# Kernel tuning notes

Measured on AMD Instinct MI355X. Metric: run time of the kernel, lower is better.

## Reference

```python
import jax, jax.numpy as jnp
import numpy as np

N, E = 50000, 500000
D_NODE, D_EDGE, N_REL, N_CLS = 128, 128, 64, 16


def setup_inputs() -> dict:
    key = jax.random.key(0)
    ks = jax.random.split(key, 16)
    cat = 2 * D_NODE + D_EDGE  # 384
    s = 0.05
    return {
        "node_features": jax.random.normal(ks[0], (N, D_NODE), jnp.float32),
        "edge_features": jax.random.normal(ks[1], (E, D_EDGE), jnp.float32),
        "edge_index": jax.random.randint(ks[2], (2, E), 0, N, jnp.int32),
        "labels_for_rel_emb": jax.random.randint(ks[3], (E,), 0, N_REL, jnp.int32),
        "rel_emb": jax.random.normal(ks[4], (N_REL, D_EDGE), jnp.float32) * s,
        "msg_W": jax.random.normal(ks[5], (D_NODE, cat), jnp.float32) * s,
        "msg_b": jnp.zeros((D_NODE,), jnp.float32),
        "gru_w_ih": jax.random.normal(ks[6], (3 * D_NODE, D_NODE), jnp.float32) * s,
        "gru_w_hh": jax.random.normal(ks[7], (3 * D_NODE, D_NODE), jnp.float32) * s,
        "gru_b_ih": jnp.zeros((3 * D_NODE,), jnp.float32),
        "gru_b_hh": jnp.zeros((3 * D_NODE,), jnp.float32),
        "cls_W1": jax.random.normal(ks[8], (D_EDGE, cat), jnp.float32) * s,
        "cls_b1": jnp.zeros((D_EDGE,), jnp.float32),
        "cls_W2": jax.random.normal(ks[9], (N_CLS, D_EDGE), jnp.float32) * s,
        "cls_b2": jnp.zeros((N_CLS,), jnp.float32),
    }


def reference(node_features, edge_features, edge_index, labels_for_rel_emb,
              rel_emb, msg_W, msg_b, gru_w_ih, gru_w_hh, gru_b_ih, gru_b_hh,
              cls_W1, cls_b1, cls_W2, cls_b2):
    src, tgt = edge_index[0], edge_index[1]
    nf = node_features
    rel_feat = rel_emb[labels_for_rel_emb]                      # [E, d_edge]
    h = jnp.concatenate([nf[src], nf[tgt], rel_feat], axis=-1)  # [E, 384]
    msg = jax.nn.gelu(h @ msg_W.T + msg_b, approximate=False)   # [E, d_node]
    agg = jax.ops.segment_sum(msg, tgt, num_segments=nf.shape[0])  # [N, d_node]
    # torch.nn.GRUCell(agg, nf)
    gi = agg @ gru_w_ih.T + gru_b_ih
    gh = nf @ gru_w_hh.T + gru_b_hh
    i_r, i_z, i_n = jnp.split(gi, 3, axis=-1)
    h_r, h_z, h_n = jnp.split(gh, 3, axis=-1)
    r = jax.nn.sigmoid(i_r + h_r)
    z = jax.nn.sigmoid(i_z + h_z)
    n = jnp.tanh(i_n + r * h_n)
    nf_u = (1.0 - z) * n + z * nf
    c = jnp.concatenate([nf_u[src], nf_u[tgt], edge_features], axis=-1)  # [E, 384]
    hc = jax.nn.gelu(c @ cls_W1.T + cls_b1, approximate=False)           # [E, d_edge]
    return hc @ cls_W2.T + cls_b2                                        # [E, num_classes]
```

## Files before the change

kernel.cpp:

```cpp
#include <hip/hip_runtime.h>
#include <math.h>

#define N_NODES 50000
#define N_EDGES 500000
#define D 128
#define CAT 384

typedef __bf16 v8bf __attribute__((ext_vector_type(8)));
typedef __bf16 v2bf __attribute__((ext_vector_type(2)));
typedef float v4f __attribute__((ext_vector_type(4)));

__device__ __forceinline__ float erf_fast(float x) {
    float ax = fabsf(x);
    float t = __builtin_amdgcn_rcpf(fmaf(0.3275911f, ax, 1.0f));
    float p = fmaf(1.061405429f, t, -1.453152027f);
    p = fmaf(p, t, 1.421413741f);
    p = fmaf(p, t, -0.284496736f);
    p = fmaf(p, t, 0.254829592f);
    p = p * t;
    float e = __expf(-ax * ax);
    float r = 1.0f - p * e;
    return copysignf(r, x);
}

__device__ __forceinline__ float gelu_fast(float x) {
    return 0.5f * x * (1.0f + erf_fast(x * 0.70710678118654752440f));
}

__device__ __forceinline__ float sigmoid_fast(float x) {
    float e = __expf(-x);
    return __builtin_amdgcn_rcpf(1.0f + e);
}

__device__ __forceinline__ float tanh_fast(float x) {
    float e = __expf(2.0f * x);
    return 1.0f - 2.0f * __builtin_amdgcn_rcpf(e + 1.0f);
}

__device__ __forceinline__ v8bf cvt8(const float* __restrict__ p) {
    float4 f0 = *(const float4*)p;
    float4 f1 = *(const float4*)(p + 4);
    v8bf r;
    r[0] = (__bf16)f0.x; r[1] = (__bf16)f0.y; r[2] = (__bf16)f0.z; r[3] = (__bf16)f0.w;
    r[4] = (__bf16)f1.x; r[5] = (__bf16)f1.y; r[6] = (__bf16)f1.z; r[7] = (__bf16)f1.w;
    return r;
}

__global__ __launch_bounds__(256) void k_cvtw(const float* __restrict__ msgW,
                                              const float* __restrict__ W1,
                                              const float* __restrict__ W2,
                                              const float* __restrict__ wih,
                                              const float* __restrict__ whh,
                                              __bf16* __restrict__ WB) {
    int i = blockIdx.x * 256 + threadIdx.x;
    float v;
    if (i < 32768) {
        int j = i >> 7, k = i & 127;
        v = (j < 128) ? msgW[j * CAT + k] : msgW[(j - 128) * CAT + 128 + k];
    } else if (i < 65536) {
        int ii = i - 32768; int j = ii >> 7, k = ii & 127;
        v = (j < 128) ? W1[j * CAT + k] : W1[(j - 128) * CAT + 128 + k];
    } else if (i < 81920) {
        int ii = i - 65536; int j = ii >> 7, k = ii & 127;
        v = W1[j * CAT + 256 + k];
    } else if (i < 83968) {
        v = W2[i - 81920];
    } else if (i < 133120) {
        v = wih[i - 83968];
    } else {
        v = whh[i - 133120];
    }
    WB[i] = (__bf16)v;
}

__global__ void k_relpart(const float* __restrict__ rel_emb,
                          const float* __restrict__ msg_W,
                          const float* __restrict__ msg_b,
                          __bf16* __restrict__ RPB) {
    int r = blockIdx.x;
    int j = threadIdx.x;
    const float* er = rel_emb + r * D;
    const float* wr = msg_W + j * CAT + 2 * D;
    float acc = msg_b[j];
    #pragma unroll 8
    for (int k = 0; k < D; ++k) acc += er[k] * wr[k];
    RPB[r * D + j] = (__bf16)acc;
}

__global__ __launch_bounds__(256) void k_proj2_f32(const float* __restrict__ in,
                                                   const __bf16* __restrict__ wb,
                                                   __bf16* __restrict__ out) {
    int t = threadIdx.x;
    int lane = t & 63, wid = t >> 6;
    int g = lane >> 4, c = lane & 15;
    int nbase = blockIdx.x * 64 + wid * 16;

    int nrow = min(nbase + c, N_NODES - 1);
    const float* ir = in + (size_t)nrow * D + g * 8;
    v8bf afrag[4];
    #pragma unroll
    for (int kc = 0; kc < 4; ++kc) afrag[kc] = cvt8(ir + kc * 32);

    #pragma unroll
    for (int half = 0; half < 2; ++half) {
        v4f acc[8];
        #pragma unroll 2
        for (int jt = 0; jt < 8; ++jt) {
            const __bf16* wr = wb + (size_t)(half * 128 + 8 * c + jt) * 128 + g * 8;
            v4f a4 = (v4f){0.f, 0.f, 0.f, 0.f};
            #pragma unroll
            for (int kc = 0; kc < 4; ++kc)
                a4 = __builtin_amdgcn_mfma_f32_16x16x32_bf16(afrag[kc], *(const v8bf*)(wr + kc * 32), a4, 0, 0, 0);
            acc[jt] = a4;
        }
        #pragma unroll
        for (int r = 0; r < 4; ++r) {
            int node = nbase + g * 4 + r;
            v8bf o;
            #pragma unroll
            for (int jt = 0; jt < 8; ++jt) o[jt] = (__bf16)acc[jt][r];
            if (node < N_NODES)
                *(v8bf*)(out + (size_t)node * 256 + half * 128 + 8 * c) = o;
        }
    }
}

__global__ __launch_bounds__(256) void k_proj2_b16(const __bf16* __restrict__ in,
                                                   const __bf16* __restrict__ wb,
                                                   __bf16* __restrict__ out) {
    int t = threadIdx.x;
    int lane = t & 63, wid = t >> 6;
    int g = lane >> 4, c = lane & 15;
    int nbase = blockIdx.x * 64 + wid * 16;

    int nrow = min(nbase + c, N_NODES - 1);
    const __bf16* ir = in + (size_t)nrow * D + g * 8;
    v8bf afrag[4];
    #pragma unroll
    for (int kc = 0; kc < 4; ++kc) afrag[kc] = *(const v8bf*)(ir + kc * 32);

    #pragma unroll
    for (int half = 0; half < 2; ++half) {
        v4f acc[8];
        #pragma unroll 2
        for (int jt = 0; jt < 8; ++jt) {
            const __bf16* wr = wb + (size_t)(half * 128 + 8 * c + jt) * 128 + g * 8;
            v4f a4 = (v4f){0.f, 0.f, 0.f, 0.f};
            #pragma unroll
            for (int kc = 0; kc < 4; ++kc)
                a4 = __builtin_amdgcn_mfma_f32_16x16x32_bf16(afrag[kc], *(const v8bf*)(wr + kc * 32), a4, 0, 0, 0);
            acc[jt] = a4;
        }
        #pragma unroll
        for (int r = 0; r < 4; ++r) {
            int node = nbase + g * 4 + r;
            v8bf o;
            #pragma unroll
            for (int jt = 0; jt < 8; ++jt) o[jt] = (__bf16)acc[jt][r];
            if (node < N_NODES)
                *(v8bf*)(out + (size_t)node * 256 + half * 128 + 8 * c) = o;
        }
    }
}

__global__ __launch_bounds__(256) void k_hist(const int* __restrict__ ei,
                                              int* __restrict__ counts) {
    int e = blockIdx.x * 256 + threadIdx.x;
    if (e < N_EDGES) atomicAdd(&counts[ei[N_EDGES + e]], 1);
}

__global__ __launch_bounds__(256) void k_scan(const int* __restrict__ counts,
                                              int* __restrict__ offsets,
                                              int* __restrict__ cursor) {
    __shared__ int part[256];
    int t = threadIdx.x;
    const int CH = 196;
    int lo = t * CH, hi = min(lo + CH, N_NODES);
    int s = 0;
    for (int i = lo; i < hi; ++i) s += counts[i];
    part[t] = s;
    __syncthreads();
    for (int d = 1; d < 256; d <<= 1) {
        int v = (t >= d) ? part[t - d] : 0;
        __syncthreads();
        part[t] += v;
        __syncthreads();
    }
    int run = (t == 0) ? 0 : part[t - 1];
    for (int i = lo; i < hi; ++i) {
        offsets[i] = run;
        cursor[i] = run;
        run += counts[i];
    }
    if (t == 255) offsets[N_NODES] = run;
}

__global__ __launch_bounds__(256) void k_scatter(const int* __restrict__ ei,
                                                 int* __restrict__ cursor,
                                                 int* __restrict__ elist) {
    int e = blockIdx.x * 256 + threadIdx.x;
    if (e < N_EDGES) {
        int slot = atomicAdd(&cursor[ei[N_EDGES + e]], 1);
        elist[slot] = e;
    }
}

__global__ __launch_bounds__(256) void k_agg(const __bf16* __restrict__ PSTB,
                                             const __bf16* __restrict__ RPB,
                                             const int* __restrict__ ei,
                                             const int* __restrict__ lab,
                                             const int* __restrict__ offsets,
                                             const int* __restrict__ elist,
                                             __bf16* __restrict__ agg) {
    int t = threadIdx.x;
    int wid = t >> 6, lane = t & 63;
    int n = blockIdx.x * 4 + wid;
    if (n >= N_NODES) return;
    int beg = offsets[n], end = offsets[n + 1];

    v2bf ptv = *(const v2bf*)(PSTB + (size_t)n * 256 + 128 + lane * 2);
    float pt0 = (float)ptv[0], pt1 = (float)ptv[1];

    float a0 = 0.f, a1 = 0.f;
    int idx = beg;
    int s_nx = 0, l_nx = 0;
    if (idx < end) { int e = elist[idx]; s_nx = ei[e]; l_nx = lab[e]; }
    while (idx < end) {
        int s = s_nx, l = l_nx;
        v2bf ps = *(const v2bf*)(PSTB + (size_t)s * 256 + lane * 2);
        v2bf rp = *(const v2bf*)(RPB + (size_t)l * D + lane * 2);
        ++idx;
        if (idx < end) { int e = elist[idx]; s_nx = ei[e]; l_nx = lab[e]; }
        a0 += gelu_fast((float)ps[0] + pt0 + (float)rp[0]);
        a1 += gelu_fast((float)ps[1] + pt1 + (float)rp[1]);
    }
    v2bf o; o[0] = (__bf16)a0; o[1] = (__bf16)a1;
    *(v2bf*)(agg + (size_t)n * D + lane * 2) = o;
}

__global__ __launch_bounds__(256) void k_gru_mfma(const __bf16* __restrict__ agg,
                                                  const float* __restrict__ nf,
                                                  const __bf16* __restrict__ WIH,
                                                  const __bf16* __restrict__ WHH,
                                                  const float* __restrict__ b_ih,
                                                  const float* __restrict__ b_hh,
                                                  __bf16* __restrict__ nfu) {
    int t = threadIdx.x;
    int lane = t & 63, wid = t >> 6;
    int g = lane >> 4, c = lane & 15;
    int nbase = blockIdx.x * 64 + wid * 16;

    int nrow = min(nbase + c, N_NODES - 1);
    const __bf16* ar = agg + (size_t)nrow * D + g * 8;
    const float* hr = nf + (size_t)nrow * D + g * 8;
    v8bf afrag[4], hfrag[4];
    #pragma unroll
    for (int kc = 0; kc < 4; ++kc) {
        afrag[kc] = *(const v8bf*)(ar + kc * 32);
        hfrag[kc] = cvt8(hr + kc * 32);
    }

    float h8[4][8];
    #pragma unroll
    for (int r = 0; r < 4; ++r) {
        int node = min(nbase + g * 4 + r, N_NODES - 1);
        float4 f0 = *(const float4*)(nf + (size_t)node * D + 8 * c);
        float4 f1 = *(const float4*)(nf + (size_t)node * D + 8 * c + 4);
        h8[r][0]=f0.x; h8[r][1]=f0.y; h8[r][2]=f0.z; h8[r][3]=f0.w;
        h8[r][4]=f1.x; h8[r][5]=f1.y; h8[r][6]=f1.z; h8[r][7]=f1.w;
    }

    v8bf o[4];
    for (int jt = 0; jt < 8; ++jt) {
        int j = 8 * c + jt;
        const __bf16* wir = WIH + (size_t)j * 128 + g * 8;
        const __bf16* whr = WHH + (size_t)j * 128 + g * 8;
        v4f a_ir = (v4f){0.f,0.f,0.f,0.f}, a_iz = a_ir, a_in = a_ir;
        v4f a_hr = a_ir, a_hz = a_ir, a_hn = a_ir;
        #pragma unroll
        for (int kc = 0; kc < 4; ++kc) {
            a_ir = __builtin_amdgcn_mfma_f32_16x16x32_bf16(afrag[kc], *(const v8bf*)(wir + kc * 32), a_ir, 0, 0, 0);
            a_iz = __builtin_amdgcn_mfma_f32_16x16x32_bf16(afrag[kc], *(const v8bf*)(wir + 128 * 128 + kc * 32), a_iz, 0, 0, 0);
            a_in = __builtin_amdgcn_mfma_f32_16x16x32_bf16(afrag[kc], *(const v8bf*)(wir + 256 * 128 + kc * 32), a_in, 0, 0, 0);
            a_hr = __builtin_amdgcn_mfma_f32_16x16x32_bf16(hfrag[kc], *(const v8bf*)(whr + kc * 32), a_hr, 0, 0, 0);
            a_hz = __builtin_amdgcn_mfma_f32_16x16x32_bf16(hfrag[kc], *(const v8bf*)(whr + 128 * 128 + kc * 32), a_hz, 0, 0, 0);
            a_hn = __builtin_amdgcn_mfma_f32_16x16x32_bf16(hfrag[kc], *(const v8bf*)(whr + 256 * 128 + kc * 32), a_hn, 0, 0, 0);
        }
        float bir = b_ih[j], biz = b_ih[128 + j], bin = b_ih[256 + j];
        float bhr = b_hh[j], bhz = b_hh[128 + j], bhn = b_hh[256 + j];
        #pragma unroll
        for (int r = 0; r < 4; ++r) {
            float irv = a_ir[r] + bir, hrv = a_hr[r] + bhr;
            float izv = a_iz[r] + biz, hzv = a_hz[r] + bhz;
            float inv = a_in[r] + bin, hnv = a_hn[r] + bhn;
            float rg = sigmoid_fast(irv + hrv);
            float zg = sigmoid_fast(izv + hzv);
            float ng = tanh_fast(inv + rg * hnv);
            o[r][jt] = (__bf16)((1.f - zg) * ng + zg * h8[r][jt]);
        }
    }
    #pragma unroll
    for (int r = 0; r < 4; ++r) {
        int node = nbase + g * 4 + r;
        if (node < N_NODES) *(v8bf*)(nfu + (size_t)node * D + 8 * c) = o[r];
    }
}

__global__ __launch_bounds__(256) void k_cls_mfma(const float* __restrict__ ef,
                                                  const __bf16* __restrict__ QSTB,
                                                  const __bf16* __restrict__ V3,
                                                  const float* __restrict__ b1,
                                                  const __bf16* __restrict__ W2B,
                                                  const float* __restrict__ b2,
                                                  const int* __restrict__ ei,
                                                  float* __restrict__ out) {
    __shared__ __align__(16) __bf16 hc_s[64][128];
    __shared__ __align__(16) __bf16 w2_s[16][128];
    int t = threadIdx.x;
    int lane = t & 63, w = t >> 6;
    int g = lane >> 4, c = lane & 15;
    int e0 = blockIdx.x * 64;
    int e_base = e0 + w * 16;

    {
        int r = t >> 4, ch = t & 15;
        v8bf v = *(const v8bf*)(W2B + r * 128 + ch * 8);
        *(v8bf*)&w2_s[r][8 * (ch ^ (r & 7))] = v;
    }

    int sr[4], tr[4];
    #pragma unroll
    for (int r = 0; r < 4; ++r) {
        int e = min(e_base + g * 4 + r, N_EDGES - 1);
        sr[r] = ei[e];
        tr[r] = ei[N_EDGES + e];
    }
    v8bf qsv[4], qtv[4];
    #pragma unroll
    for (int r = 0; r < 4; ++r) {
        qsv[r] = *(const v8bf*)(QSTB + (size_t)sr[r] * 256 + 8 * c);
        qtv[r] = *(const v8bf*)(QSTB + (size_t)tr[r] * 256 + 128 + 8 * c);
    }
    float4 b1a = *(const float4*)(b1 + 8 * c);
    float4 b1b = *(const float4*)(b1 + 8 * c + 4);
    float b1r[8] = {b1a.x, b1a.y, b1a.z, b1a.w, b1b.x, b1b.y, b1b.z, b1b.w};

    int er = min(e_base + c, N_EDGES - 1);
    const float* efr = ef + (size_t)er * D + g * 8;
    v8bf afrag[4];
    #pragma unroll
    for (int kc = 0; kc < 4; ++kc) afrag[kc] = cvt8(efr + kc * 32);

    v4f acc[8];
    #pragma unroll 2
    for (int jt = 0; jt < 8; ++jt) {
        const __bf16* wr = V3 + (size_t)(8 * c + jt) * 128 + g * 8;
        v4f a4 = (v4f){0.f, 0.f, 0.f, 0.f};
        #pragma unroll
        for (int kc = 0; kc < 4; ++kc)
            a4 = __builtin_amdgcn_mfma_f32_16x16x32_bf16(afrag[kc], *(const v8bf*)(wr + kc * 32), a4, 0, 0, 0);
        acc[jt] = a4;
    }

    #pragma unroll
    for (int r = 0; r < 4; ++r) {
        int el = w * 16 + g * 4 + r;
        v8bf o;
        #pragma unroll
        for (int jt = 0; jt < 8; ++jt) {
            float v = acc[jt][r] + (float)qsv[r][jt] + (float)qtv[r][jt] + b1r[jt];
            o[jt] = (__bf16)gelu_fast(v);
        }
        *(v8bf*)&hc_s[el][8 * (c ^ (el & 7))] = o;
    }
    __syncthreads();

    v4f acc2 = (v4f){0.f, 0.f, 0.f, 0.f};
    int arow = w * 16 + c;
    #pragma unroll
    for (int kc = 0; kc < 4; ++kc) {
        int ch = g + 4 * kc;
        v8bf aa = *(const v8bf*)&hc_s[arow][8 * (ch ^ (c & 7))];
        v8bf bb = *(const v8bf*)&w2_s[c][8 * (ch ^ (c & 7))];
        acc2 = __builtin_amdgcn_mfma_f32_16x16x32_bf16(aa, bb, acc2, 0, 0, 0);
    }
    float b2c = b2[c];
    #pragma unroll
    for (int r = 0; r < 4; ++r) {
        int e = e_base + g * 4 + r;
        if (e < N_EDGES) out[(size_t)e * 16 + c] = acc2[r] + b2c;
    }
}

extern "C" void kernel_launch(void* const* d_in, const int* in_sizes, int n_in,
                              void* d_out, int out_size, void* d_ws, size_t ws_size,
                              hipStream_t stream) {
    const float* nf   = (const float*)d_in[0];
    const float* ef   = (const float*)d_in[1];
    const int*   ei   = (const int*)d_in[2];
    const int*   lab  = (const int*)d_in[3];
    const float* rel  = (const float*)d_in[4];
    const float* msgW = (const float*)d_in[5];
    const float* msgb = (const float*)d_in[6];
    const float* wih  = (const float*)d_in[7];
    const float* whh  = (const float*)d_in[8];
    const float* bih  = (const float*)d_in[9];
    const float* bhh  = (const float*)d_in[10];
    const float* W1   = (const float*)d_in[11];
    const float* b1   = (const float*)d_in[12];
    const float* W2   = (const float*)d_in[13];
    const float* b2   = (const float*)d_in[14];
    float* out = (float*)d_out;

    char* ws = (char*)d_ws;
    __bf16* WB      = (__bf16*)(ws);
    __bf16* RPB     = (__bf16*)(ws + 524288);
    int*    offsets = (int*)(ws + 1048576);
    int*    counts  = (int*)(ws + 1310720);
    int*    cursor  = (int*)(ws + 1572864);
    int*    elist   = (int*)(ws + 1835008);
    __bf16* PSTB    = (__bf16*)(ws + 4194304);
    __bf16* AGG     = (__bf16*)(ws + 33554432);
    __bf16* NFUB    = (__bf16*)(ws + 50331648);
    __bf16* QSTB    = PSTB;

    __bf16* WP1 = WB;
    __bf16* WQ1 = WB + 32768;
    __bf16* V3  = WB + 65536;
    __bf16* W2B = WB + 81920;
    __bf16* WIH = WB + 83968;
    __bf16* WHH = WB + 133120;

    int nblk = (N_NODES + 63) / 64;
    int eblk = (N_EDGES + 255) / 256;

    k_cvtw<<<712, 256, 0, stream>>>(msgW, W1, W2, wih, whh, WB);
    k_relpart<<<64, 128, 0, stream>>>(rel, msgW, msgb, RPB);
    hipMemsetAsync(counts, 0, N_NODES * sizeof(int), stream);
    k_hist<<<eblk, 256, 0, stream>>>(ei, counts);
    k_proj2_f32<<<nblk, 256, 0, stream>>>(nf, WP1, PSTB);
    k_scan<<<1, 256, 0, stream>>>(counts, offsets, cursor);
    k_scatter<<<eblk, 256, 0, stream>>>(ei, cursor, elist);
    k_agg<<<(N_NODES + 3) / 4, 256, 0, stream>>>(PSTB, RPB, ei, lab, offsets, elist, AGG);
    k_gru_mfma<<<nblk, 256, 0, stream>>>(AGG, nf, WIH, WHH, bih, bhh, NFUB);
    k_proj2_b16<<<nblk, 256, 0, stream>>>(NFUB, WQ1, QSTB);
    k_cls_mfma<<<(N_EDGES + 63) / 64, 256, 0, stream>>>(ef, QSTB, V3, b1, W2B, b2, ei, out);
}
```

Before: 591.9 us.

## Fuse setup kernels, deepen agg prefetch, streamline classifier kernel loads and sync

Merges the weight conversion, relation-part projection and histogram kernels into one launch, which removes two kernel launches and their gaps. The aggregation loop now runs a two-stage software pipeline: it fetches edge indices two steps ahead and gathered feature rows one step ahead, so gather latency is better hidden. The classifier kernel issues its edge-feature loads at the start, fully unrolls the first MFMA loop, and reads W2 straight from global memory instead of staging it in shared memory. That drops a block-wide barrier, relying on each wave reading back only the shared-memory rows it wrote itself. Costs are higher register pressure and repeated global loads of W2 per wave.

```diff
diff --git a/kernel.cpp b/kernel.cpp
--- a/kernel.cpp
+++ b/kernel.cpp
@@ -46,45 +46,52 @@
     return r;
 }
 
-__global__ __launch_bounds__(256) void k_cvtw(const float* __restrict__ msgW,
-                                              const float* __restrict__ W1,
-                                              const float* __restrict__ W2,
-                                              const float* __restrict__ wih,
-                                              const float* __restrict__ whh,
-                                              __bf16* __restrict__ WB) {
-    int i = blockIdx.x * 256 + threadIdx.x;
-    float v;
-    if (i < 32768) {
-        int j = i >> 7, k = i & 127;
-        v = (j < 128) ? msgW[j * CAT + k] : msgW[(j - 128) * CAT + 128 + k];
-    } else if (i < 65536) {
-        int ii = i - 32768; int j = ii >> 7, k = ii & 127;
-        v = (j < 128) ? W1[j * CAT + k] : W1[(j - 128) * CAT + 128 + k];
-    } else if (i < 81920) {
-        int ii = i - 65536; int j = ii >> 7, k = ii & 127;
-        v = W1[j * CAT + 256 + k];
-    } else if (i < 83968) {
-        v = W2[i - 81920];
-    } else if (i < 133120) {
-        v = wih[i - 83968];
+__global__ __launch_bounds__(256) void k_pre(const float* __restrict__ msgW,
+                                             const float* __restrict__ W1,
+                                             const float* __restrict__ W2,
+                                             const float* __restrict__ wih,
+                                             const float* __restrict__ whh,
+                                             __bf16* __restrict__ WB,
+                                             const float* __restrict__ rel_emb,
+                                             const float* __restrict__ msg_b,
+                                             __bf16* __restrict__ RPB,
+                                             const int* __restrict__ ei,
+                                             int* __restrict__ counts) {
+    int bid = blockIdx.x;
+    int t = threadIdx.x;
+    if (bid < 712) {
+        int i = bid * 256 + t;
+        float v;
+        if (i < 32768) {
+            int j = i >> 7, k = i & 127;
+            v = (j < 128) ? msgW[j * CAT + k] : msgW[(j - 128) * CAT + 128 + k];
+        } else if (i < 65536) {
+            int ii = i - 32768; int j = ii >> 7, k = ii & 127;
+            v = (j < 128) ? W1[j * CAT + k] : W1[(j - 128) * CAT + 128 + k];
+        } else if (i < 81920) {
+            int ii = i - 65536; int j = ii >> 7, k = ii & 127;
+            v = W1[j * CAT + 256 + k];
+        } else if (i < 83968) {
+            v = W2[i - 81920];
+        } else if (i < 133120) {
+            v = wih[i - 83968];
+        } else {
+            v = whh[i - 133120];
+        }
+        WB[i] = (__bf16)v;
+    } else if (bid < 744) {
+        int r = (bid - 712) * 2 + (t >> 7);
+        int j = t & 127;
+        const float* er = rel_emb + r * D;
+        const float* wr = msgW + j * CAT + 2 * D;
+        float acc = msg_b[j];
+        #pragma unroll 8
+        for (int k = 0; k < D; ++k) acc += er[k] * wr[k];
+        RPB[r * D + j] = (__bf16)acc;
     } else {
-        v = whh[i - 133120];
-    }
-    WB[i] = (__bf16)v;
-}
-
-__global__ void k_relpart(const float* __restrict__ rel_emb,
-                          const float* __restrict__ msg_W,
-                          const float* __restrict__ msg_b,
-                          __bf16* __restrict__ RPB) {
-    int r = blockIdx.x;
-    int j = threadIdx.x;
-    const float* er = rel_emb + r * D;
-    const float* wr = msg_W + j * CAT + 2 * D;
-    float acc = msg_b[j];
-    #pragma unroll 8
-    for (int k = 0; k < D; ++k) acc += er[k] * wr[k];
-    RPB[r * D + j] = (__bf16)acc;
+        int e = (bid - 744) * 256 + t;
+        if (e < N_EDGES) atomicAdd(&counts[ei[N_EDGES + e]], 1);
+    }
 }
 
 __global__ __launch_bounds__(256) void k_proj2_f32(const float* __restrict__ in,
@@ -161,12 +168,6 @@
                 *(v8bf*)(out + (size_t)node * 256 + half * 128 + 8 * c) = o;
         }
     }
-}
-
-__global__ __launch_bounds__(256) void k_hist(const int* __restrict__ ei,
-                                              int* __restrict__ counts) {
-    int e = blockIdx.x * 256 + threadIdx.x;
-    if (e < N_EDGES) atomicAdd(&counts[ei[N_EDGES + e]], 1);
 }
 
 __global__ __launch_bounds__(256) void k_scan(const int* __restrict__ counts,
@@ -222,15 +223,25 @@
     float pt0 = (float)ptv[0], pt1 = (float)ptv[1];
 
     float a0 = 0.f, a1 = 0.f;
-    int idx = beg;
-    int s_nx = 0, l_nx = 0;
-    if (idx < end) { int e = elist[idx]; s_nx = ei[e]; l_nx = lab[e]; }
-    while (idx < end) {
-        int s = s_nx, l = l_nx;
-        v2bf ps = *(const v2bf*)(PSTB + (size_t)s * 256 + lane * 2);
-        v2bf rp = *(const v2bf*)(RPB + (size_t)l * D + lane * 2);
-        ++idx;
-        if (idx < end) { int e = elist[idx]; s_nx = ei[e]; l_nx = lab[e]; }
+    v2bf ps0 = {}, rp0 = {};
+    int s1 = 0, l1 = 0;
+    if (beg < end) {
+        int e = elist[beg]; int s = ei[e]; int l = lab[e];
+        ps0 = *(const v2bf*)(PSTB + (size_t)s * 256 + lane * 2);
+        rp0 = *(const v2bf*)(RPB + (size_t)l * D + lane * 2);
+    }
+    if (beg + 1 < end) {
+        int e = elist[beg + 1]; s1 = ei[e]; l1 = lab[e];
+    }
+    for (int idx = beg; idx < end; ++idx) {
+        v2bf ps = ps0, rp = rp0;
+        if (idx + 1 < end) {
+            ps0 = *(const v2bf*)(PSTB + (size_t)s1 * 256 + lane * 2);
+            rp0 = *(const v2bf*)(RPB + (size_t)l1 * D + lane * 2);
+        }
+        if (idx + 2 < end) {
+            int e = elist[idx + 2]; s1 = ei[e]; l1 = lab[e];
+        }
         a0 += gelu_fast((float)ps[0] + pt0 + (float)rp[0]);
         a1 += gelu_fast((float)ps[1] + pt1 + (float)rp[1]);
     }
@@ -315,17 +326,19 @@
                                                   const int* __restrict__ ei,
                                                   float* __restrict__ out) {
     __shared__ __align__(16) __bf16 hc_s[64][128];
-    __shared__ __align__(16) __bf16 w2_s[16][128];
     int t = threadIdx.x;
     int lane = t & 63, w = t >> 6;
     int g = lane >> 4, c = lane & 15;
     int e0 = blockIdx.x * 64;
     int e_base = e0 + w * 16;
 
-    {
-        int r = t >> 4, ch = t & 15;
-        v8bf v = *(const v8bf*)(W2B + r * 128 + ch * 8);
-        *(v8bf*)&w2_s[r][8 * (ch ^ (r & 7))] = v;
+    int er = min(e_base + c, N_EDGES - 1);
+    const float* efr = ef + (size_t)er * D + g * 8;
+    float4 efraw[8];
+    #pragma unroll
+    for (int kc = 0; kc < 4; ++kc) {
+        efraw[2 * kc]     = *(const float4*)(efr + kc * 32);
+        efraw[2 * kc + 1] = *(const float4*)(efr + kc * 32 + 4);
     }
 
     int sr[4], tr[4];
@@ -345,14 +358,18 @@
     float4 b1b = *(const float4*)(b1 + 8 * c + 4);
     float b1r[8] = {b1a.x, b1a.y, b1a.z, b1a.w, b1b.x, b1b.y, b1b.z, b1b.w};
 
-    int er = min(e_base + c, N_EDGES - 1);
-    const float* efr = ef + (size_t)er * D + g * 8;
     v8bf afrag[4];
     #pragma unroll
-    for (int kc = 0; kc < 4; ++kc) afrag[kc] = cvt8(efr + kc * 32);
+    for (int kc = 0; kc < 4; ++kc) {
+        v8bf a;
+        float4 f0 = efraw[2 * kc], f1 = efraw[2 * kc + 1];
+        a[0] = (__bf16)f0.x; a[1] = (__bf16)f0.y; a[2] = (__bf16)f0.z; a[3] = (__bf16)f0.w;
+        a[4] = (__bf16)f1.x; a[5] = (__bf16)f1.y; a[6] = (__bf16)f1.z; a[7] = (__bf16)f1.w;
+        afrag[kc] = a;
+    }
 
     v4f acc[8];
-    #pragma unroll 2
+    #pragma unroll
     for (int jt = 0; jt < 8; ++jt) {
         const __bf16* wr = V3 + (size_t)(8 * c + jt) * 128 + g * 8;
         v4f a4 = (v4f){0.f, 0.f, 0.f, 0.f};
@@ -373,7 +390,6 @@
         }
         *(v8bf*)&hc_s[el][8 * (c ^ (el & 7))] = o;
     }
-    __syncthreads();
 
     v4f acc2 = (v4f){0.f, 0.f, 0.f, 0.f};
     int arow = w * 16 + c;
@@ -381,7 +397,7 @@
     for (int kc = 0; kc < 4; ++kc) {
         int ch = g + 4 * kc;
         v8bf aa = *(const v8bf*)&hc_s[arow][8 * (ch ^ (c & 7))];
-        v8bf bb = *(const v8bf*)&w2_s[c][8 * (ch ^ (c & 7))];
+        v8bf bb = *(const v8bf*)(W2B + c * 128 + ch * 8);
         acc2 = __builtin_amdgcn_mfma_f32_16x16x32_bf16(aa, bb, acc2, 0, 0, 0);
     }
     float b2c = b2[c];
@@ -434,10 +450,9 @@
     int nblk = (N_NODES + 63) / 64;
     int eblk = (N_EDGES + 255) / 256;
 
-    k_cvtw<<<712, 256, 0, stream>>>(msgW, W1, W2, wih, whh, WB);
-    k_relpart<<<64, 128, 0, stream>>>(rel, msgW, msgb, RPB);
     hipMemsetAsync(counts, 0, N_NODES * sizeof(int), stream);
-    k_hist<<<eblk, 256, 0, stream>>>(ei, counts);
+    k_pre<<<744 + eblk, 256, 0, stream>>>(msgW, W1, W2, wih, whh, WB,
+                                          rel, msgb, RPB, ei, counts);
     k_proj2_f32<<<nblk, 256, 0, stream>>>(nf, WP1, PSTB);
     k_scan<<<1, 256, 0, stream>>>(counts, offsets, cursor);
     k_scatter<<<eblk, 256, 0, stream>>>(ei, cursor, elist);
```

Result: no change. 590.8 us (-0.2%).
